# Performance work log

Hardware: AMD Instinct MI355X
Metric: run time of the kernel (lower is better)

The kernel has to match this reference:

```python
import jax, jax.numpy as jnp
from jax import lax
import numpy as np


def _greedy_match(s):
    """Sequential greedy assignment on a single [N, N] score matrix.
    Mirrors Binary.forward for the n1=n2=None (square) case:
    repeat N times: pick global argmax, zero its row and column in the
    working copy, set perm[row, col] = 1.
    """
    N = s.shape[0]

    def step(carry, _):
        s_tmp, perm = carry
        idx = jnp.argmax(s_tmp)          # flat argmax over N*N
        r = idx // N
        c = idx % N
        s_tmp = s_tmp.at[r, :].set(0.0).at[:, c].set(0.0)
        perm = perm.at[r, c].set(1.0)
        return (s_tmp, perm), None

    (_, perm), _ = lax.scan(step, (s, jnp.zeros_like(s)), None, length=N)
    return perm


def setup_inputs() -> dict:
    key = jax.random.key(0)
    B, N = 256, 512
    s = jax.random.uniform(key, (B, N, N), dtype=jnp.float32)
    return {"s": s}


def reference(s):
    # vmap over batch; each batch element runs an independent sequential
    # greedy matching (the data-dependent part is the length-N scan).
    return jax.vmap(_greedy_match)(s)
```

## Files before the change

kernel.cpp:

```cpp
#include <hip/hip_runtime.h>

#define NN 512
#define BATCH 256
#define T 8
#define ATH 40

typedef unsigned long long u64;
typedef unsigned u32;
typedef unsigned char u8;
typedef unsigned short u16;

#define DEADK 512ull
#define LIVEMIN (1ull << 32)
#define UNKNOWN 0xFFFFu

__device__ __forceinline__ u64 fm(u64 a, u64 b) {
    return (u64)__double_as_longlong(fmax(__longlong_as_double((long long)a),
                                          __longlong_as_double((long long)b)));
}
__device__ __forceinline__ u64 fmn(u64 a, u64 b) {
    return (u64)__double_as_longlong(fmin(__longlong_as_double((long long)a),
                                          __longlong_as_double((long long)b)));
}

#define DPP_FMAX64(k, ctrl) do {                                              \
    int _lo = (int)(u32)(k); int _hi = (int)((k) >> 32);                      \
    int _olo = __builtin_amdgcn_update_dpp(_lo, _lo, ctrl, 0xf, 0xf, false);  \
    int _ohi = __builtin_amdgcn_update_dpp(_hi, _hi, ctrl, 0xf, 0xf, false);  \
    u64 _o = ((u64)(u32)_ohi << 32) | (u32)_olo;                              \
    (k) = fm((k), _o);                                                        \
} while (0)

#define WAVE_FMAX64(k) do {                                                   \
    DPP_FMAX64(k, 0x111); DPP_FMAX64(k, 0x112); DPP_FMAX64(k, 0x114);         \
    DPP_FMAX64(k, 0x118); DPP_FMAX64(k, 0x142); DPP_FMAX64(k, 0x143);         \
} while (0)

__device__ __forceinline__ u64 readlane64(u64 k, int l) {
    u32 lo = (u32)__builtin_amdgcn_readlane((int)(u32)k, l);
    u32 hi = (u32)__builtin_amdgcn_readlane((int)(k >> 32), l);
    return ((u64)hi << 32) | lo;
}

__device__ __forceinline__ u64 amsel(int w, u64 a0, u64 a1, u64 a2, u64 a3,
                                     u64 a4, u64 a5, u64 a6, u64 a7) {
    u64 x01 = (w & 1) ? a1 : a0;
    u64 x23 = (w & 1) ? a3 : a2;
    u64 x45 = (w & 1) ? a5 : a4;
    u64 x67 = (w & 1) ? a7 : a6;
    u64 y0 = (w & 2) ? x23 : x01;
    u64 y1 = (w & 2) ? x67 : x45;
    return (w & 4) ? y1 : y0;
}

#define INS8(X, A0, A1, A2, A3, A4, A5, A6, A7) do {                          \
    u64 _x = (X), _n;                                                         \
    _n = fm(A0, _x); _x = fmn(A0, _x); A0 = _n;                               \
    _n = fm(A1, _x); _x = fmn(A1, _x); A1 = _n;                               \
    _n = fm(A2, _x); _x = fmn(A2, _x); A2 = _n;                               \
    _n = fm(A3, _x); _x = fmn(A3, _x); A3 = _n;                               \
    _n = fm(A4, _x); _x = fmn(A4, _x); A4 = _n;                               \
    _n = fm(A5, _x); _x = fmn(A5, _x); A5 = _n;                               \
    _n = fm(A6, _x); _x = fmn(A6, _x); A6 = _n;                               \
    A7 = fm(A7, _x);                                                          \
} while (0)

#define ALIVE_C(cc) ((amsel((int)(cc) >> 6, am0,am1,am2,am3,am4,am5,am6,am7)  \
                      >> ((cc) & 63)) & 1ull)
#define ALIVE_R(rr) ((amsel((int)(rr) >> 6, ar0,ar1,ar2,ar3,ar4,ar5,ar6,ar7)  \
                      >> ((rr) & 63)) & 1ull)
#define SETK(RS, VAL) do {                                                    \
        const int rsl_ = (RS) & 63, rsj_ = (RS) >> 6;                         \
        const bool mn_ = (lane == rsl_);                                      \
        k0 = (mn_ && rsj_ == 0) ? (VAL) : k0;                                 \
        k1 = (mn_ && rsj_ == 1) ? (VAL) : k1;                                 \
        k2 = (mn_ && rsj_ == 2) ? (VAL) : k2;                                 \
        k3 = (mn_ && rsj_ == 3) ? (VAL) : k3;                                 \
        k4 = (mn_ && rsj_ == 4) ? (VAL) : k4;                                 \
        k5 = (mn_ && rsj_ == 5) ? (VAL) : k5;                                 \
        k6 = (mn_ && rsj_ == 6) ? (VAL) : k6;                                 \
        k7 = (mn_ && rsj_ == 7) ? (VAL) : k7;                                 \
    } while (0)

#define COLDROW(RR, NKVAR) do {                                               \
        const float* rp_ = sb + (size_t)(RR) * NN;                            \
        const float4 fa_ = *(const float4*)(rp_ + 4 * lane);                  \
        const float4 fv_ = *(const float4*)(rp_ + 256 + 4 * lane);            \
        const int sh_ = (4 * lane) & 63; const int wq_ = lane >> 4;           \
        u64 xlo_ = (wq_ == 0) ? am0 : (wq_ == 1) ? am1 : (wq_ == 2) ? am2 : am3; \
        u64 xhi_ = (wq_ == 0) ? am4 : (wq_ == 1) ? am5 : (wq_ == 2) ? am6 : am7; \
        const u32 al8_ = ((u32)(xlo_ >> sh_) & 0xFu)                          \
                       | (((u32)(xhi_ >> sh_) & 0xFu) << 4);                  \
        u64 e0_ = (al8_ & 1u)   ? ((((u64)__float_as_uint(fa_.x) + 1) << 9) | (u32)(511 - (4*lane+0))) : 0; \
        u64 e1_ = (al8_ & 2u)   ? ((((u64)__float_as_uint(fa_.y) + 1) << 9) | (u32)(511 - (4*lane+1))) : 0; \
        u64 e2_ = (al8_ & 4u)   ? ((((u64)__float_as_uint(fa_.z) + 1) << 9) | (u32)(511 - (4*lane+2))) : 0; \
        u64 e3_ = (al8_ & 8u)   ? ((((u64)__float_as_uint(fa_.w) + 1) << 9) | (u32)(511 - (4*lane+3))) : 0; \
        u64 e4_ = (al8_ & 16u)  ? ((((u64)__float_as_uint(fv_.x) + 1) << 9) | (u32)(511 - (256+4*lane+0))) : 0; \
        u64 e5_ = (al8_ & 32u)  ? ((((u64)__float_as_uint(fv_.y) + 1) << 9) | (u32)(511 - (256+4*lane+1))) : 0; \
        u64 e6_ = (al8_ & 64u)  ? ((((u64)__float_as_uint(fv_.z) + 1) << 9) | (u32)(511 - (256+4*lane+2))) : 0; \
        u64 e7_ = (al8_ & 128u) ? ((((u64)__float_as_uint(fv_.w) + 1) << 9) | (u32)(511 - (256+4*lane+3))) : 0; \
        u64 n0_ = fm(e0_, e1_), n1_ = fm(e2_, e3_);                           \
        u64 n2_ = fm(e4_, e5_), n3_ = fm(e6_, e7_);                           \
        n0_ = fm(n0_, n1_); n2_ = fm(n2_, n3_);                               \
        u64 bw_ = fm(n0_, n2_);                                               \
        WAVE_FMAX64(bw_);                                                     \
        bw_ = readlane64(bw_, 63);                                            \
        const int wc_ = 511 - (int)(bw_ & 511);                               \
        NKVAR = ((bw_ >> 9) << 32)                                            \
              | ((u64)(u32)(512 - (RR)) << 16) | (u32)wc_;                    \
        if (lane == 0)                                                        \
            rl[RR][7] = (((bw_ >> 9) - 1ull) << 32) | (u32)wc_;               \
    } while (0)

__global__ __launch_bounds__(256) void build_top(const float* __restrict__ s,
                                                 float* __restrict__ out) {
    const int wave = threadIdx.x >> 6;
    const int lane = threadIdx.x & 63;
    const int row_g = blockIdx.x * 4 + wave;
    const int b = row_g >> 9;
    const int r = row_g & (NN - 1);
    const float* rp = s + (size_t)row_g * NN;
    u64* dst = (u64*)(out + (size_t)b * NN * NN) + (size_t)r * T;

    const float4 a  = *(const float4*)(rp + 4 * lane);
    const float4 c2 = *(const float4*)(rp + 256 + 4 * lane);

    u64 kk0 = (((u64)__float_as_uint(a.x)  + 1) << 9) | (u32)(511 - (4*lane + 0));
    u64 kk1 = (((u64)__float_as_uint(a.y)  + 1) << 9) | (u32)(511 - (4*lane + 1));
    u64 kk2 = (((u64)__float_as_uint(a.z)  + 1) << 9) | (u32)(511 - (4*lane + 2));
    u64 kk3 = (((u64)__float_as_uint(a.w)  + 1) << 9) | (u32)(511 - (4*lane + 3));
    u64 kk4 = (((u64)__float_as_uint(c2.x) + 1) << 9) | (u32)(511 - (256 + 4*lane + 0));
    u64 kk5 = (((u64)__float_as_uint(c2.y) + 1) << 9) | (u32)(511 - (256 + 4*lane + 1));
    u64 kk6 = (((u64)__float_as_uint(c2.z) + 1) << 9) | (u32)(511 - (256 + 4*lane + 2));
    u64 kk7 = (((u64)__float_as_uint(c2.w) + 1) << 9) | (u32)(511 - (256 + 4*lane + 3));

    #pragma unroll
    for (int t = 0; t < T; ++t) {
        u64 m0 = fm(kk0, kk1), m1 = fm(kk2, kk3);
        u64 m2 = fm(kk4, kk5), m3 = fm(kk6, kk7);
        m0 = fm(m0, m1); m2 = fm(m2, m3);
        u64 bk = fm(m0, m2);
        WAVE_FMAX64(bk);
        bk = readlane64(bk, 63);

        const int wcol = 511 - (int)(bk & 511);
        const u32 vb = (u32)(bk >> 9) - 1u;
        if (lane == 0) dst[t] = ((u64)vb << 32) | (u32)wcol;

        const int owner = (wcol & 255) >> 2;
        const int slot  = ((wcol >> 8) << 2) | (wcol & 3);
        if (lane == owner) {
            kk0 = (slot == 0) ? 0 : kk0;  kk1 = (slot == 1) ? 0 : kk1;
            kk2 = (slot == 2) ? 0 : kk2;  kk3 = (slot == 3) ? 0 : kk3;
            kk4 = (slot == 4) ? 0 : kk4;  kk5 = (slot == 5) ? 0 : kk5;
            kk6 = (slot == 6) ? 0 : kk6;  kk7 = (slot == 7) ? 0 : kk7;
        }
    }
}

__global__ __launch_bounds__(256) void build_col(const float* __restrict__ s,
                                                 float* __restrict__ out) {
    const int b = blockIdx.x >> 3;
    const int cbase = (blockIdx.x & 7) * 64;
    const int t = threadIdx.x;
    const int ct = t & 63, q = t >> 6;

    __shared__ float tile[64][65];
    __shared__ u64 mrg[64][4][8];

    const float* sb = s + (size_t)b * NN * NN;

    u64 t0 = 0, t1 = 0, t2 = 0, t3 = 0, t4 = 0, t5 = 0, t6 = 0, t7 = 0;

    for (int ch = 0; ch < 8; ++ch) {
        const int rbase = ch * 64;
        #pragma unroll
        for (int i = 0; i < 16; ++i) {
            const int rr = q + 4 * i;
            tile[rr][ct] = sb[(size_t)(rbase + rr) * NN + cbase + ct];
        }
        __syncthreads();
        #pragma unroll
        for (int i = 0; i < 16; ++i) {
            const int rr = rbase + q * 16 + i;
            const float v = tile[q * 16 + i][ct];
            const u64 x = (((u64)__float_as_uint(v) + 1) << 9) | (u32)(511 - rr);
            INS8(x, t0, t1, t2, t3, t4, t5, t6, t7);
        }
        __syncthreads();
    }

    mrg[ct][q][0] = t0;  mrg[ct][q][1] = t1;  mrg[ct][q][2] = t2;
    mrg[ct][q][3] = t3;  mrg[ct][q][4] = t4;  mrg[ct][q][5] = t5;
    mrg[ct][q][6] = t6;  mrg[ct][q][7] = t7;
    __syncthreads();

    if (t < 64) {
        u64 m0 = 0, m1 = 0, m2 = 0, m3 = 0, m4 = 0, m5 = 0, m6 = 0, m7 = 0;
        #pragma unroll
        for (int qq = 0; qq < 4; ++qq)
            #pragma unroll
            for (int ii = 0; ii < 8; ++ii) {
                const u64 x = mrg[t][qq][ii];
                INS8(x, m0, m1, m2, m3, m4, m5, m6, m7);
            }
        u64* dst = (u64*)(out + (size_t)b * NN * NN) + (size_t)NN * T
                 + (size_t)(cbase + t) * T;
        dst[0] = m0; dst[1] = m1; dst[2] = m2; dst[3] = m3;
        dst[4] = m4; dst[5] = m5; dst[6] = m6; dst[7] = m7;
    }
}

__global__ __launch_bounds__(256) void greedy_A(const float* __restrict__ s,
                                                float* __restrict__ out,
                                                u32* __restrict__ ws_mat) {
    __shared__ __align__(16) u64 rl[NN][9];
    __shared__ __align__(16) u64 cl[NN][9];
    __shared__ __align__(16) u64 keysL[NN];
    __shared__ u32 colh[NN];
    __shared__ u8 aliveR[NN];
    __shared__ u8 aliveC[NN];
    __shared__ u16 match16[NN];
    __shared__ int cntW[4];

    const int tid = threadIdx.x;
    const int w = tid >> 6, lane = tid & 63;
    const int b = blockIdx.x;
    const float* sb = s + (size_t)b * NN * NN;
    float* ob = out + (size_t)b * NN * NN;
    u64* st = (u64*)ob + 8192;

    {
        const ulonglong2* src = (const ulonglong2*)ob;
        #pragma unroll
        for (int i = 0; i < 8; ++i) {
            const int i2 = tid + 256 * i;
            const ulonglong2 vR = src[i2];
            const ulonglong2 vC = src[2048 + i2];
            const int idx = i2 * 2;
            rl[idx >> 3][idx & 7] = vR.x;  rl[idx >> 3][(idx & 7) + 1] = vR.y;
            cl[idx >> 3][idx & 7] = vC.x;  cl[idx >> 3][(idx & 7) + 1] = vC.y;
        }
    }
    if (tid < 128) {
        ((u32*)aliveR)[tid] = 0x01010101u;
        ((u32*)aliveC)[tid] = 0x01010101u;
    }
    match16[tid] = 0; match16[tid + 256] = 0;
    __syncthreads();
    #pragma unroll
    for (int i = 0; i < 2; ++i) {
        const int r = tid + 256 * i;
        const u64 e = rl[r][0];
        keysL[r] = (((e >> 32) + 1ull) << 32)
                 | ((u64)(u32)(512 - r) << 16) | (e & 511ull);
        colh[r] = 511u - ((u32)cl[r][0] & 511u);
    }
    __syncthreads();

    u64 am0 = ~0ull, am1 = ~0ull, am2 = ~0ull, am3 = ~0ull,
        am4 = ~0ull, am5 = ~0ull, am6 = ~0ull, am7 = ~0ull;
    u64 ar0 = ~0ull, ar1 = ~0ull, ar2 = ~0ull, ar3 = ~0ull,
        ar4 = ~0ull, ar5 = ~0ull, ar6 = ~0ull, ar7 = ~0ull;

    int alive = NN;

    #pragma unroll 1
    for (int round = 0; round < 64; ++round) {
        int part = 0;
        #pragma unroll
        for (int j = 0; j < 2; ++j) {
            const int row = 128 * w + 64 * j + lane;
            const u64 kj = keysL[row];
            const u32 cc = (u32)kj & 511u;
            const bool hit = (kj >= LIVEMIN) && (colh[cc] == (u32)row);
            part += (int)__builtin_popcountll(__ballot(hit));
            if (hit) {
                match16[row] = (u16)cc;
                aliveC[cc] = 0;
                aliveR[row] = 0;
                keysL[row] = DEADK;
            }
        }
        if (lane == 0) cntW[w] = part;
        __syncthreads();
        const int cnt = cntW[0] + cntW[1] + cntW[2] + cntW[3];
        if (cnt == 0) break;
        alive -= cnt;

        am0 = __ballot(aliveC[lane] != 0);        am1 = __ballot(aliveC[64 + lane] != 0);
        am2 = __ballot(aliveC[128 + lane] != 0);  am3 = __ballot(aliveC[192 + lane] != 0);
        am4 = __ballot(aliveC[256 + lane] != 0);  am5 = __ballot(aliveC[320 + lane] != 0);
        am6 = __ballot(aliveC[384 + lane] != 0);  am7 = __ballot(aliveC[448 + lane] != 0);
        ar0 = __ballot(aliveR[lane] != 0);        ar1 = __ballot(aliveR[64 + lane] != 0);
        ar2 = __ballot(aliveR[128 + lane] != 0);  ar3 = __ballot(aliveR[192 + lane] != 0);
        ar4 = __ballot(aliveR[256 + lane] != 0);  ar5 = __ballot(aliveR[320 + lane] != 0);
        ar6 = __ballot(aliveR[384 + lane] != 0);  ar7 = __ballot(aliveR[448 + lane] != 0);

        if (alive <= ATH) break;

        u32 coldR = 0;
        #pragma unroll
        for (int j = 0; j < 2; ++j) {
            const int row = 128 * w + 64 * j + lane;
            const u64 kj = keysL[row];
            if (kj >= LIVEMIN && !ALIVE_C((u32)kj & 511u)) {
                const u64 f0 = rl[row][0], f1 = rl[row][1], f2 = rl[row][2];
                const u64 f3 = rl[row][3], f4 = rl[row][4], f5 = rl[row][5];
                const u64 f6 = rl[row][6], f7 = rl[row][7];
                const u64 a0 = ALIVE_C((u32)f0 & 511u);
                const u64 a1 = ALIVE_C((u32)f1 & 511u);
                const u64 a2 = ALIVE_C((u32)f2 & 511u);
                const u64 a3 = ALIVE_C((u32)f3 & 511u);
                const u64 a4 = ALIVE_C((u32)f4 & 511u);
                const u64 a5 = ALIVE_C((u32)f5 & 511u);
                const u64 a6 = ALIVE_C((u32)f6 & 511u);
                const u64 a7 = ALIVE_C((u32)f7 & 511u);
                u64 sel = 0;
                sel = a7 ? f7 : sel; sel = a6 ? f6 : sel;
                sel = a5 ? f5 : sel; sel = a4 ? f4 : sel;
                sel = a3 ? f3 : sel; sel = a2 ? f2 : sel;
                sel = a1 ? f1 : sel; sel = a0 ? f0 : sel;
                if (a0 | a1 | a2 | a3 | a4 | a5 | a6 | a7) {
                    keysL[row] = ((sel >> 32) + 1ull) << 32
                               | ((u64)(u32)(512 - row) << 16) | (sel & 511ull);
                } else coldR |= 1u << j;
            }
        }
        u64 mk = __ballot(coldR != 0u);
        while (mk) {
            const int l = (int)__builtin_ctzll(mk); mk &= mk - 1;
            u32 lm = (u32)__builtin_amdgcn_readlane((int)coldR, l);
            while (lm) {
                const int jj = (int)__builtin_ctz(lm); lm &= lm - 1;
                const int r = 128 * w + 64 * jj + l;
                u64 nkc;
                COLDROW(r, nkc);
                if (lane == 0) keysL[r] = nkc;
            }
        }

        #pragma unroll
        for (int j = 0; j < 2; ++j) {
            const int c = 128 * w + 64 * j + lane;
            const u32 chv = colh[c];
            if (aliveC[c] && chv != UNKNOWN && !ALIVE_R(chv)) {
                const u64 g0 = cl[c][0], g1 = cl[c][1], g2 = cl[c][2];
                const u64 g3 = cl[c][3], g4 = cl[c][4], g5 = cl[c][5];
                const u64 g6 = cl[c][6], g7 = cl[c][7];
                const u64 b0 = ALIVE_R(511u - ((u32)g0 & 511u));
                const u64 b1 = ALIVE_R(511u - ((u32)g1 & 511u));
                const u64 b2 = ALIVE_R(511u - ((u32)g2 & 511u));
                const u64 b3 = ALIVE_R(511u - ((u32)g3 & 511u));
                const u64 b4 = ALIVE_R(511u - ((u32)g4 & 511u));
                const u64 b5 = ALIVE_R(511u - ((u32)g5 & 511u));
                const u64 b6 = ALIVE_R(511u - ((u32)g6 & 511u));
                const u64 b7 = ALIVE_R(511u - ((u32)g7 & 511u));
                u64 sel = 0;
                sel = b7 ? g7 : sel; sel = b6 ? g6 : sel;
                sel = b5 ? g5 : sel; sel = b4 ? g4 : sel;
                sel = b3 ? g3 : sel; sel = b2 ? g2 : sel;
                sel = b1 ? g1 : sel; sel = b0 ? g0 : sel;
                colh[c] = (b0 | b1 | b2 | b3 | b4 | b5 | b6 | b7)
                        ? (511u - ((u32)sel & 511u)) : UNKNOWN;
            }
        }
        __syncthreads();
    }

    __syncthreads();
    st[tid] = keysL[tid];
    st[tid + 256] = keysL[tid + 256];
    if (tid < 8)
        st[512 + tid] = amsel(tid, am0, am1, am2, am3, am4, am5, am6, am7);
    ws_mat[b * 256 + tid] = ((const u32*)match16)[tid];
}

__global__ __launch_bounds__(64) void greedy_B(const float* __restrict__ s,
                                               const float* __restrict__ out,
                                               u32* __restrict__ ws_mat) {
    __shared__ __align__(16) u64 rl[NN][8];
    __shared__ u16 match16[NN];

    const int b = blockIdx.x;
    const int lane = threadIdx.x;
    const float* sb = s + (size_t)b * NN * NN;
    const float* ob = out + (size_t)b * NN * NN;
    const u64* st = (const u64*)ob + 8192;

    {
        const ulonglong2* src = (const ulonglong2*)ob;
        ulonglong2* dstl = (ulonglong2*)&rl[0][0];
        #pragma unroll
        for (int j = 0; j < 32; ++j)
            dstl[lane + 64 * j] = src[lane + 64 * j];
    }
    {
        u32* m32 = (u32*)match16;
        #pragma unroll
        for (int i = 0; i < 4; ++i)
            m32[lane + 64 * i] = ws_mat[b * 256 + lane + 64 * i];
    }

    u64 am0 = st[512], am1 = st[513], am2 = st[514], am3 = st[515];
    u64 am4 = st[516], am5 = st[517], am6 = st[518], am7 = st[519];

    u64 k0 = st[lane];        u64 k1 = st[lane + 64];
    u64 k2 = st[lane + 128];  u64 k3 = st[lane + 192];
    u64 k4 = st[lane + 256];  u64 k5 = st[lane + 320];
    u64 k6 = st[lane + 384];  u64 k7 = st[lane + 448];

    int done = NN;
    done -= (int)__builtin_popcountll(__ballot(k0 >= LIVEMIN));
    done -= (int)__builtin_popcountll(__ballot(k1 >= LIVEMIN));
    done -= (int)__builtin_popcountll(__ballot(k2 >= LIVEMIN));
    done -= (int)__builtin_popcountll(__ballot(k3 >= LIVEMIN));
    done -= (int)__builtin_popcountll(__ballot(k4 >= LIVEMIN));
    done -= (int)__builtin_popcountll(__ballot(k5 >= LIVEMIN));
    done -= (int)__builtin_popcountll(__ballot(k6 >= LIVEMIN));
    done -= (int)__builtin_popcountll(__ballot(k7 >= LIVEMIN));

    #pragma unroll 1
    while (done < NN) {
        u64 m0 = fm(k0, k1), m1 = fm(k2, k3), m2 = fm(k4, k5), m3 = fm(k6, k7);
        m0 = fm(m0, m1); m2 = fm(m2, m3);
        u64 bk = fm(m0, m2);
        WAVE_FMAX64(bk);
        const u32 lo = (u32)__builtin_amdgcn_readlane((int)(u32)bk, 63);
        const int cstar = (int)(lo & 511u);
        const int rstar = 512 - (int)((lo >> 16) & 1023u);

        const u64 e = rl[rstar][lane & 7];
        const int cw = cstar >> 6;
        const u64 aw = amsel(cw, am0, am1, am2, am3, am4, am5, am6, am7);
        const bool valid = ((aw >> (cstar & 63)) & 1ull) != 0ull;

        u64 nk;
        if (valid) {
            if (lane == 0) match16[rstar] = (u16)cstar;
            const u64 nb = ~(1ull << (cstar & 63));
            am0 = (cw == 0) ? (am0 & nb) : am0;  am1 = (cw == 1) ? (am1 & nb) : am1;
            am2 = (cw == 2) ? (am2 & nb) : am2;  am3 = (cw == 3) ? (am3 & nb) : am3;
            am4 = (cw == 4) ? (am4 & nb) : am4;  am5 = (cw == 5) ? (am5 & nb) : am5;
            am6 = (cw == 6) ? (am6 & nb) : am6;  am7 = (cw == 7) ? (am7 & nb) : am7;
            nk = DEADK;
            ++done;
        } else {
            const int c = (int)(e & 511u);
            const u64 w = amsel(c >> 6, am0, am1, am2, am3, am4, am5, am6, am7);
            const bool al = ((w >> (c & 63)) & 1ull) != 0ull;
            const u64 mask = __ballot(al) & 0xFFull;
            if (mask) {
                const u64 es = readlane64(e, (int)__builtin_ctzll(mask));
                nk = (((es >> 32) + 1ull) << 32)
                   | ((u64)(u32)(512 - rstar) << 16) | (es & 511ull);
            } else {
                COLDROW(rstar, nk);
            }
        }
        SETK(rstar, nk);
    }

    {
        const u32* m32 = (const u32*)match16;
        #pragma unroll
        for (int i = 0; i < 4; ++i)
            ws_mat[b * 256 + lane + 64 * i] = m32[lane + 64 * i];
    }
}

__global__ __launch_bounds__(256) void write_out(const u32* __restrict__ ws_mat,
                                                 float* __restrict__ out) {
    const int gid = blockIdx.x * 256 + threadIdx.x;
    const int b = gid >> 16;
    const int rem = gid & 65535;
    const int row = rem >> 7;
    const int quad = rem & 127;
    const u32 w = ws_mat[b * 256 + (row >> 1)];
    const int c = (int)((w >> (16 * (row & 1))) & 0xFFFFu);
    float4 f;
    f.x = (c == quad * 4 + 0) ? 1.0f : 0.0f;
    f.y = (c == quad * 4 + 1) ? 1.0f : 0.0f;
    f.z = (c == quad * 4 + 2) ? 1.0f : 0.0f;
    f.w = (c == quad * 4 + 3) ? 1.0f : 0.0f;
    ((float4*)out)[gid] = f;
}

extern "C" void kernel_launch(void* const* d_in, const int* in_sizes, int n_in,
                              void* d_out, int out_size, void* d_ws, size_t ws_size,
                              hipStream_t stream) {
    const float* s = (const float*)d_in[0];
    float* out = (float*)d_out;
    u32* ws_mat = (u32*)d_ws;

    build_top<<<dim3(BATCH * NN / 4), dim3(256), 0, stream>>>(s, out);
    build_col<<<dim3(BATCH * 8), dim3(256), 0, stream>>>(s, out);
    greedy_A<<<dim3(BATCH), dim3(256), 0, stream>>>(s, out, ws_mat);
    greedy_B<<<dim3(BATCH), dim3(64), 0, stream>>>(s, out, ws_mat);
    write_out<<<dim3(BATCH * 256), dim3(256), 0, stream>>>(ws_mat, out);
}
```

Baseline: 306.9 us.

## Replace per-row wave top-8 reduction with shared-memory tiled insertion-sort kernel

The per-row top-8 builder, which ran one wave per row doing eight full-wave max reductions, is replaced by a kernel shaped like the column builder. It stages 64x64 tiles through shared memory, keeps per-thread top-8 lists with INS8 insertion, then merges four partial lists per row. The goal is to remove the repeated cross-lane reductions and the large block count. In exchange it adds transposed shared-memory reads, serial insertion work per thread and a merge step.

```diff
diff --git a/kernel.cpp b/kernel.cpp
--- a/kernel.cpp
+++ b/kernel.cpp
@@ -112,49 +112,61 @@
             rl[RR][7] = (((bw_ >> 9) - 1ull) << 32) | (u32)wc_;               \
     } while (0)
 
-__global__ __launch_bounds__(256) void build_top(const float* __restrict__ s,
+__global__ __launch_bounds__(256) void build_row(const float* __restrict__ s,
                                                  float* __restrict__ out) {
-    const int wave = threadIdx.x >> 6;
-    const int lane = threadIdx.x & 63;
-    const int row_g = blockIdx.x * 4 + wave;
-    const int b = row_g >> 9;
-    const int r = row_g & (NN - 1);
-    const float* rp = s + (size_t)row_g * NN;
-    u64* dst = (u64*)(out + (size_t)b * NN * NN) + (size_t)r * T;
-
-    const float4 a  = *(const float4*)(rp + 4 * lane);
-    const float4 c2 = *(const float4*)(rp + 256 + 4 * lane);
-
-    u64 kk0 = (((u64)__float_as_uint(a.x)  + 1) << 9) | (u32)(511 - (4*lane + 0));
-    u64 kk1 = (((u64)__float_as_uint(a.y)  + 1) << 9) | (u32)(511 - (4*lane + 1));
-    u64 kk2 = (((u64)__float_as_uint(a.z)  + 1) << 9) | (u32)(511 - (4*lane + 2));
-    u64 kk3 = (((u64)__float_as_uint(a.w)  + 1) << 9) | (u32)(511 - (4*lane + 3));
-    u64 kk4 = (((u64)__float_as_uint(c2.x) + 1) << 9) | (u32)(511 - (256 + 4*lane + 0));
-    u64 kk5 = (((u64)__float_as_uint(c2.y) + 1) << 9) | (u32)(511 - (256 + 4*lane + 1));
-    u64 kk6 = (((u64)__float_as_uint(c2.z) + 1) << 9) | (u32)(511 - (256 + 4*lane + 2));
-    u64 kk7 = (((u64)__float_as_uint(c2.w) + 1) << 9) | (u32)(511 - (256 + 4*lane + 3));
-
-    #pragma unroll
-    for (int t = 0; t < T; ++t) {
-        u64 m0 = fm(kk0, kk1), m1 = fm(kk2, kk3);
-        u64 m2 = fm(kk4, kk5), m3 = fm(kk6, kk7);
-        m0 = fm(m0, m1); m2 = fm(m2, m3);
-        u64 bk = fm(m0, m2);
-        WAVE_FMAX64(bk);
-        bk = readlane64(bk, 63);
-
-        const int wcol = 511 - (int)(bk & 511);
-        const u32 vb = (u32)(bk >> 9) - 1u;
-        if (lane == 0) dst[t] = ((u64)vb << 32) | (u32)wcol;
-
-        const int owner = (wcol & 255) >> 2;
-        const int slot  = ((wcol >> 8) << 2) | (wcol & 3);
-        if (lane == owner) {
-            kk0 = (slot == 0) ? 0 : kk0;  kk1 = (slot == 1) ? 0 : kk1;
-            kk2 = (slot == 2) ? 0 : kk2;  kk3 = (slot == 3) ? 0 : kk3;
-            kk4 = (slot == 4) ? 0 : kk4;  kk5 = (slot == 5) ? 0 : kk5;
-            kk6 = (slot == 6) ? 0 : kk6;  kk7 = (slot == 7) ? 0 : kk7;
-        }
+    const int b = blockIdx.x >> 3;
+    const int rbase = (blockIdx.x & 7) * 64;
+    const int t = threadIdx.x;
+    const int ct = t & 63, q = t >> 6;
+
+    __shared__ float tile[64][65];
+    __shared__ u64 mrg[64][4][8];
+
+    const float* sb = s + (size_t)b * NN * NN;
+
+    u64 t0 = 0, t1 = 0, t2 = 0, t3 = 0, t4 = 0, t5 = 0, t6 = 0, t7 = 0;
+
+    for (int ch = 0; ch < 8; ++ch) {
+        const int cbase = ch * 64;
+        #pragma unroll
+        for (int i = 0; i < 16; ++i) {
+            const int rr = q + 4 * i;
+            tile[rr][ct] = sb[(size_t)(rbase + rr) * NN + cbase + ct];
+        }
+        __syncthreads();
+        #pragma unroll
+        for (int i = 0; i < 16; ++i) {
+            const int cc = cbase + 16 * q + i;
+            const float v = tile[ct][16 * q + i];
+            const u64 x = (((u64)__float_as_uint(v) + 1) << 9) | (u32)(511 - cc);
+            INS8(x, t0, t1, t2, t3, t4, t5, t6, t7);
+        }
+        __syncthreads();
+    }
+
+    mrg[ct][q][0] = t0;  mrg[ct][q][1] = t1;  mrg[ct][q][2] = t2;
+    mrg[ct][q][3] = t3;  mrg[ct][q][4] = t4;  mrg[ct][q][5] = t5;
+    mrg[ct][q][6] = t6;  mrg[ct][q][7] = t7;
+    __syncthreads();
+
+    if (t < 64) {
+        u64 m0 = 0, m1 = 0, m2 = 0, m3 = 0, m4 = 0, m5 = 0, m6 = 0, m7 = 0;
+        #pragma unroll
+        for (int qq = 0; qq < 4; ++qq)
+            #pragma unroll
+            for (int ii = 0; ii < 8; ++ii) {
+                const u64 x = mrg[t][qq][ii];
+                INS8(x, m0, m1, m2, m3, m4, m5, m6, m7);
+            }
+        u64* dst = (u64*)(out + (size_t)b * NN * NN) + (size_t)(rbase + t) * T;
+        dst[0] = (((m0 >> 9) - 1ull) << 32) | (u32)(511 - (int)(m0 & 511));
+        dst[1] = (((m1 >> 9) - 1ull) << 32) | (u32)(511 - (int)(m1 & 511));
+        dst[2] = (((m2 >> 9) - 1ull) << 32) | (u32)(511 - (int)(m2 & 511));
+        dst[3] = (((m3 >> 9) - 1ull) << 32) | (u32)(511 - (int)(m3 & 511));
+        dst[4] = (((m4 >> 9) - 1ull) << 32) | (u32)(511 - (int)(m4 & 511));
+        dst[5] = (((m5 >> 9) - 1ull) << 32) | (u32)(511 - (int)(m5 & 511));
+        dst[6] = (((m6 >> 9) - 1ull) << 32) | (u32)(511 - (int)(m6 & 511));
+        dst[7] = (((m7 >> 9) - 1ull) << 32) | (u32)(511 - (int)(m7 & 511));
     }
 }
 
@@ -493,7 +505,7 @@
     float* out = (float*)d_out;
     u32* ws_mat = (u32*)d_ws;
 
-    build_top<<<dim3(BATCH * NN / 4), dim3(256), 0, stream>>>(s, out);
+    build_row<<<dim3(BATCH * 8), dim3(256), 0, stream>>>(s, out);
     build_col<<<dim3(BATCH * 8), dim3(256), 0, stream>>>(s, out);
     greedy_A<<<dim3(BATCH), dim3(256), 0, stream>>>(s, out, ws_mat);
     greedy_B<<<dim3(BATCH), dim3(64), 0, stream>>>(s, out, ws_mat);
```

Result: faster. 295.1 us (-3.8%).
